# Kernel optimization log

Hardware: AMD Instinct MI355X
Metric: run time of the kernel (lower is better)

The kernel has to match this reference:

```python
import jax, jax.numpy as jnp
import numpy as np

B, S, M, D, H, L, FF = 2, 1024, 1024, 512, 8, 4, 2048
HD = D // H  # head dim 64
EPS = 1e-6   # fast_transformers linear-attention eps
LN_EPS = 1e-5


def setup_inputs() -> dict:
    key = jax.random.key(0)
    keys = iter(jax.random.split(key, 64))
    def w(shape, s=0.02):
        return jax.random.normal(next(keys), shape, dtype=jnp.float32) * s
    inp = {
        "memory": jax.random.normal(next(keys), (B, M, D), dtype=jnp.float32),
        "target": jax.random.normal(next(keys), (B, S, D), dtype=jnp.float32),
    }
    for p in ("sa", "ca"):
        for n in ("q", "k", "v", "o"):
            inp[f"{p}_W{n}"] = w((L, D, D))
            inp[f"{p}_b{n}"] = jnp.zeros((L, D), jnp.float32)
    inp["ff_W1"] = w((L, D, FF)); inp["ff_b1"] = jnp.zeros((L, FF), jnp.float32)
    inp["ff_W2"] = w((L, FF, D)); inp["ff_b2"] = jnp.zeros((L, D), jnp.float32)
    for n in ("ln1", "ln2", "ln3"):
        inp[f"{n}_g"] = jnp.ones((L, D), jnp.float32)
        inp[f"{n}_b"] = jnp.zeros((L, D), jnp.float32)
    inp["lnf_g"] = jnp.ones((D,), jnp.float32)
    inp["lnf_b"] = jnp.zeros((D,), jnp.float32)
    return inp


def _ln(x, g, b):
    m = x.mean(-1, keepdims=True)
    v = ((x - m) ** 2).mean(-1, keepdims=True)
    return (x - m) / jnp.sqrt(v + LN_EPS) * g + b


def _phi(x):  # elu feature map: elu(x) + 1
    return jax.nn.elu(x) + 1.0


def _heads(x, W, b):  # [b,s,D] -> [b,s,H,HD]
    y = x @ W + b
    return y.reshape(y.shape[0], y.shape[1], H, HD)


def _causal_linear_attn(q, k, v):
    # q,k already feature-mapped. cumulative KV state per step.
    kv = jnp.cumsum(jnp.einsum('bshd,bshm->bshdm', k, v), axis=1)  # [B,S,H,HD,HD]
    z = jnp.cumsum(k, axis=1)                                      # [B,S,H,HD]
    num = jnp.einsum('bshd,bshdm->bshm', q, kv)
    den = jnp.einsum('bshd,bshd->bsh', q, z) + EPS
    return num / den[..., None]


def _cross_linear_attn(q, k, v):
    kv = jnp.einsum('bmhd,bmhv->bhdv', k, v)  # [B,H,HD,HD]
    z = k.sum(axis=1)                          # [B,H,HD]
    num = jnp.einsum('bshd,bhdv->bshv', q, kv)
    den = jnp.einsum('bshd,bhd->bsh', q, z) + EPS
    return num / den[..., None]


def reference(memory, target,
              sa_Wq, sa_bq, sa_Wk, sa_bk, sa_Wv, sa_bv, sa_Wo, sa_bo,
              ca_Wq, ca_bq, ca_Wk, ca_bk, ca_Wv, ca_bv, ca_Wo, ca_bo,
              ff_W1, ff_b1, ff_W2, ff_b2,
              ln1_g, ln1_b, ln2_g, ln2_b, ln3_g, ln3_b, lnf_g, lnf_b):
    x = target
    for i in range(L):
        # causal linear self-attention
        q = _phi(_heads(x, sa_Wq[i], sa_bq[i]))
        k = _phi(_heads(x, sa_Wk[i], sa_bk[i]))
        v = _heads(x, sa_Wv[i], sa_bv[i])
        a = _causal_linear_attn(q, k, v).reshape(B, S, D) @ sa_Wo[i] + sa_bo[i]
        x = _ln(x + a, ln1_g[i], ln1_b[i])
        # linear cross-attention over memory
        q = _phi(_heads(x, ca_Wq[i], ca_bq[i]))
        k = _phi(_heads(memory, ca_Wk[i], ca_bk[i]))
        v = _heads(memory, ca_Wv[i], ca_bv[i])
        a = _cross_linear_attn(q, k, v).reshape(B, S, D) @ ca_Wo[i] + ca_bo[i]
        x = _ln(x + a, ln2_g[i], ln2_b[i])
        # gelu FFN
        y = jax.nn.gelu(x @ ff_W1[i] + ff_b1[i], approximate=False) @ ff_W2[i] + ff_b2[i]
        x = _ln(x + y, ln3_g[i], ln3_b[i])
    return _ln(x, lnf_g, lnf_b)
```

## Files before the change

kernel.cpp:

```cpp
#include <hip/hip_runtime.h>
#include <hip/hip_bf16.h>
#include <math.h>


typedef unsigned short u16;
typedef __bf16 bf16x8 __attribute__((ext_vector_type(8)));
typedef float f32x4v __attribute__((ext_vector_type(4)));
typedef long long i64;

#define DEVI __device__ __forceinline__

DEVI float bf2f(u16 u) { return __uint_as_float(((unsigned)u) << 16); }
DEVI u16 f2bf(float f) {
  unsigned u = __float_as_uint(f);
  u += 0x7FFFu + ((u >> 16) & 1u);
  return (u16)(u >> 16);
}

struct P8i { const float* p[8]; };
struct P8o { u16* p[8]; };

__global__ __launch_bounds__(256) void transpose_b8(P8i in, P8o out)
{
  __shared__ float tile[64 * 65];
  const int m = blockIdx.z;
  const int set = m >> 2, layer = m & 3;
  const float* src = in.p[set] + (size_t)layer * 512 * 512;
  u16* dst = out.p[set] + (size_t)layer * 512 * 512;
  const int n0 = blockIdx.x * 64, k0 = blockIdx.y * 64;
  const int t = threadIdx.x;
#pragma unroll
  for (int p = 0; p < 16; ++p) {
    const int e = t + p * 256;
    const int lk = e >> 6, ln = e & 63;
    tile[lk * 65 + ln] = src[(size_t)(k0 + lk) * 512 + n0 + ln];
  }
  __syncthreads();
#pragma unroll
  for (int p = 0; p < 16; ++p) {
    const int e = t + p * 256;
    const int ln = e >> 6, lk = e & 63;
    dst[(size_t)(n0 + ln) * 512 + k0 + lk] = f2bf(tile[lk * 65 + ln]);
  }
}

__global__ __launch_bounds__(256) void transpose_f2b(
    const float* __restrict__ in, u16* __restrict__ out, int K, int N)
{
  __shared__ float tile[64 * 65];
  const size_t mat = (size_t)blockIdx.z * K * N;
  const int n0 = blockIdx.x * 64, k0 = blockIdx.y * 64;
  const int t = threadIdx.x;
#pragma unroll
  for (int p = 0; p < 16; ++p) {
    const int e = t + p * 256;
    const int lk = e >> 6, ln = e & 63;
    tile[lk * 65 + ln] = in[mat + (size_t)(k0 + lk) * N + n0 + ln];
  }
  __syncthreads();
#pragma unroll
  for (int p = 0; p < 16; ++p) {
    const int e = t + p * 256;
    const int ln = e >> 6, lk = e & 63;
    out[mat + (size_t)(n0 + ln) * K + k0 + lk] = f2bf(tile[lk * 65 + ln]);
  }
}

__global__ __launch_bounds__(256) void cast_dual(
    const float* __restrict__ in, float* __restrict__ fout, u16* __restrict__ bout)
{
  const int i = blockIdx.x * 256 + threadIdx.x;
  const float4 a = ((const float4*)in)[i * 2];
  const float4 b = ((const float4*)in)[i * 2 + 1];
  if (fout) {
    ((float4*)fout)[i * 2] = a;
    ((float4*)fout)[i * 2 + 1] = b;
  }
  ((ushort4*)bout)[i * 2]     = make_ushort4(f2bf(a.x), f2bf(a.y), f2bf(a.z), f2bf(a.w));
  ((ushort4*)bout)[i * 2 + 1] = make_ushort4(f2bf(b.x), f2bf(b.y), f2bf(b.z), f2bf(b.w));
}

template<int CDT>
__global__ __launch_bounds__(256, 4) void gemm64(
    const u16* __restrict__ A0, const u16* __restrict__ A1, const u16* __restrict__ A2,
    const u16* __restrict__ W0, const u16* __restrict__ W1, const u16* __restrict__ W2,
    const float* __restrict__ b0, const float* __restrict__ b1, const float* __restrict__ b2,
    void* __restrict__ C0, void* __restrict__ C1, void* __restrict__ C2,
    int acts, int N, int K, int lda, int ldw, int lognyb,
    i64 zA, i64 zW, i64 zB, i64 zC, int biasAllZ)
{
  constexpr int LDT = 72;
  __shared__ __align__(16) u16 As[2][64 * LDT];
  __shared__ __align__(16) u16 Bs[2][64 * LDT];
  const int tid = threadIdx.x;
  const int by = blockIdx.y;
  const int z = blockIdx.z;
  const int seg = by >> lognyb;
  const int ny = by & ((1 << lognyb) - 1);
  const u16* A = (seg == 0 ? A0 : (seg == 1 ? A1 : A2)) + (size_t)z * zA;
  const u16* W = (seg == 0 ? W0 : (seg == 1 ? W1 : W2)) + (size_t)z * zW;
  const float* bias = (seg == 0 ? b0 : (seg == 1 ? b1 : b2)) + (size_t)z * zB;
  void* Cv = seg == 0 ? C0 : (seg == 1 ? C1 : C2);
  const int act = (acts >> (2 * seg)) & 3;
  const bool dobias = biasAllZ || (z == 0);

  const int bm0 = blockIdx.x * 64, bn0 = ny * 64;
  const int lane = tid & 63, wid = tid >> 6;
  const int wr = wid >> 1, wc = wid & 1;
  const int l15 = lane & 15, lg = lane >> 4;
  const int srow = tid >> 2, scg = (tid & 3) * 16;
  const u16* Ap = A + (size_t)(bm0 + srow) * lda + scg;
  const u16* Wp = W + (size_t)(bn0 + srow) * ldw + scg;

  uint4 ra0 = *(const uint4*)(Ap);
  uint4 ra1 = *(const uint4*)(Ap + 8);
  uint4 rb0 = *(const uint4*)(Wp);
  uint4 rb1 = *(const uint4*)(Wp + 8);
  *(uint4*)&As[0][srow * LDT + scg]     = ra0;
  *(uint4*)&As[0][srow * LDT + scg + 8] = ra1;
  *(uint4*)&Bs[0][srow * LDT + scg]     = rb0;
  *(uint4*)&Bs[0][srow * LDT + scg + 8] = rb1;
  __syncthreads();

  f32x4v acc[2][2] = {};
  int cur = 0;
  for (int k0 = 0; k0 < K; k0 += 64) {
    const bool more = (k0 + 64 < K);
    if (more) {
      ra0 = *(const uint4*)(Ap + k0 + 64);
      ra1 = *(const uint4*)(Ap + k0 + 72);
      rb0 = *(const uint4*)(Wp + k0 + 64);
      rb1 = *(const uint4*)(Wp + k0 + 72);
    }
    bf16x8 af[2][2], bw[2][2];
#pragma unroll
    for (int kk = 0; kk < 2; ++kk) {
#pragma unroll
      for (int mm = 0; mm < 2; ++mm)
        af[kk][mm] = *(const bf16x8*)&As[cur][(wr * 32 + mm * 16 + l15) * LDT + kk * 32 + lg * 8];
#pragma unroll
      for (int nn = 0; nn < 2; ++nn)
        bw[kk][nn] = *(const bf16x8*)&Bs[cur][(wc * 32 + nn * 16 + l15) * LDT + kk * 32 + lg * 8];
    }
#pragma unroll
    for (int kk = 0; kk < 2; ++kk)
#pragma unroll
      for (int mm = 0; mm < 2; ++mm)
#pragma unroll
        for (int nn = 0; nn < 2; ++nn)
          acc[mm][nn] = __builtin_amdgcn_mfma_f32_16x16x32_bf16(af[kk][mm], bw[kk][nn], acc[mm][nn], 0, 0, 0);
    if (more) {
      *(uint4*)&As[cur ^ 1][srow * LDT + scg]     = ra0;
      *(uint4*)&As[cur ^ 1][srow * LDT + scg + 8] = ra1;
      *(uint4*)&Bs[cur ^ 1][srow * LDT + scg]     = rb0;
      *(uint4*)&Bs[cur ^ 1][srow * LDT + scg + 8] = rb1;
    }
    __syncthreads();
    cur ^= 1;
  }
#pragma unroll
  for (int nn = 0; nn < 2; ++nn) {
    const int col = bn0 + wc * 32 + nn * 16 + l15;
    const float bv = dobias ? bias[col] : 0.f;
#pragma unroll
    for (int mm = 0; mm < 2; ++mm) {
#pragma unroll
      for (int r = 0; r < 4; ++r) {
        const int row = bm0 + wr * 32 + mm * 16 + lg * 4 + r;
        float v = acc[mm][nn][r] + bv;
        if (act == 1) v = v > 0.f ? v + 1.f : __expf(v);
        else if (act == 2) v = 0.5f * v * (1.f + erff(v * 0.70710678f));
        const size_t idx = (size_t)row * N + col + (size_t)z * zC;
        if (CDT == 0) ((float*)Cv)[idx] = v;
        else          ((u16*)Cv)[idx] = f2bf(v);
      }
    }
  }
}

__global__ __launch_bounds__(256) void lin_chunk_mfma(
    const u16* __restrict__ kbuf, const u16* __restrict__ vbuf,
    float* __restrict__ KVc, float* __restrict__ zc)
{
  constexpr int LDT = 72;
  __shared__ __align__(16) u16 Kt[64 * LDT];
  __shared__ __align__(16) u16 Vt[64 * LDT];
  const int c = blockIdx.x, bh = blockIdx.y, zl = blockIdx.z;
  kbuf += (size_t)zl * 2048 * 512;
  vbuf += (size_t)zl * 2048 * 512;
  KVc  += (size_t)zl * 16 * 16 * 4096;
  zc   += (size_t)zl * 16 * 16 * 64;
  const int b = bh >> 3, h = bh & 7;
  const int t = threadIdx.x;
  const size_t rowbase = (size_t)(b * 1024 + c * 64);
  const int sp = t >> 4, colq = (t & 15) * 4;
#pragma unroll
  for (int pp = 0; pp < 2; ++pp) {
    const int s0 = pp * 32 + 2 * sp;
    const ushort4 ka = *(const ushort4*)&kbuf[(rowbase + s0) * 512 + h * 64 + colq];
    const ushort4 kb_ = *(const ushort4*)&kbuf[(rowbase + s0 + 1) * 512 + h * 64 + colq];
    const ushort4 va = *(const ushort4*)&vbuf[(rowbase + s0) * 512 + h * 64 + colq];
    const ushort4 vb_ = *(const ushort4*)&vbuf[(rowbase + s0 + 1) * 512 + h * 64 + colq];
    *(unsigned*)&Kt[(colq + 0) * LDT + s0] = (unsigned)ka.x | ((unsigned)kb_.x << 16);
    *(unsigned*)&Kt[(colq + 1) * LDT + s0] = (unsigned)ka.y | ((unsigned)kb_.y << 16);
    *(unsigned*)&Kt[(colq + 2) * LDT + s0] = (unsigned)ka.z | ((unsigned)kb_.z << 16);
    *(unsigned*)&Kt[(colq + 3) * LDT + s0] = (unsigned)ka.w | ((unsigned)kb_.w << 16);
    *(unsigned*)&Vt[(colq + 0) * LDT + s0] = (unsigned)va.x | ((unsigned)vb_.x << 16);
    *(unsigned*)&Vt[(colq + 1) * LDT + s0] = (unsigned)va.y | ((unsigned)vb_.y << 16);
    *(unsigned*)&Vt[(colq + 2) * LDT + s0] = (unsigned)va.z | ((unsigned)vb_.z << 16);
    *(unsigned*)&Vt[(colq + 3) * LDT + s0] = (unsigned)va.w | ((unsigned)vb_.w << 16);
  }
  __syncthreads();
  {
    const int zd = t >> 2, zg = t & 3;
    float zp = 0.f;
#pragma unroll
    for (int ss = 0; ss < 16; ++ss) zp += bf2f(Kt[zd * LDT + zg * 16 + ss]);
    zp += __shfl_xor(zp, 1, 64);
    zp += __shfl_xor(zp, 2, 64);
    if (zg == 0) zc[(size_t)(bh * 16 + c) * 64 + zd] = zp;
  }
  const int lane = t & 63, wid = t >> 6;
  const int wr = wid >> 1, wc = wid & 1;
  const int l15 = lane & 15, lg = lane >> 4;
  bf16x8 av[2][2], bk[2][2];
#pragma unroll
  for (int kk = 0; kk < 2; ++kk) {
#pragma unroll
    for (int mm = 0; mm < 2; ++mm)
      av[kk][mm] = *(const bf16x8*)&Vt[(wr * 32 + mm * 16 + l15) * LDT + kk * 32 + lg * 8];
#pragma unroll
    for (int nn = 0; nn < 2; ++nn)
      bk[kk][nn] = *(const bf16x8*)&Kt[(wc * 32 + nn * 16 + l15) * LDT + kk * 32 + lg * 8];
  }
  f32x4v acc[2][2] = {};
#pragma unroll
  for (int kk = 0; kk < 2; ++kk)
#pragma unroll
    for (int mm = 0; mm < 2; ++mm)
#pragma unroll
      for (int nn = 0; nn < 2; ++nn)
        acc[mm][nn] = __builtin_amdgcn_mfma_f32_16x16x32_bf16(av[kk][mm], bk[kk][nn], acc[mm][nn], 0, 0, 0);
  float* kvout = KVc + (size_t)(bh * 16 + c) * 4096;
#pragma unroll
  for (int mm = 0; mm < 2; ++mm)
#pragma unroll
    for (int r = 0; r < 4; ++r) {
      const int row = wr * 32 + mm * 16 + lg * 4 + r;
#pragma unroll
      for (int nn = 0; nn < 2; ++nn) {
        const int col = wc * 32 + nn * 16 + l15;
        kvout[row * 64 + col] = acc[mm][nn][r];
      }
    }
}

__global__ __launch_bounds__(256) void sa_apply_mfma(
    const u16* __restrict__ qbuf, const u16* __restrict__ kbuf,
    const u16* __restrict__ vbuf, const float* __restrict__ KVc,
    const float* __restrict__ zc, u16* __restrict__ out)
{
  constexpr int LDT = 72;
  __shared__ __align__(16) u16 Qs[64 * LDT];
  __shared__ __align__(16) u16 Ks[64 * LDT];
  __shared__ __align__(16) u16 Vt[64 * LDT];
  __shared__ __align__(16) u16 Ps[64 * LDT];
  __shared__ __align__(16) u16 KVs[64 * LDT];
  __shared__ float zp[64];
  __shared__ float den1[2][64];
  __shared__ float den2[64];
  const int c = blockIdx.x, bh = blockIdx.y;
  const int b = bh >> 3, h = bh & 7;
  const int t = threadIdx.x;
  const size_t rowbase = (size_t)(b * 1024 + c * 64);
  {
    const int srow = t >> 2, scg = (t & 3) * 16;
    *(uint4*)&Qs[srow * LDT + scg]     = *(const uint4*)&qbuf[(rowbase + srow) * 512 + h * 64 + scg];
    *(uint4*)&Qs[srow * LDT + scg + 8] = *(const uint4*)&qbuf[(rowbase + srow) * 512 + h * 64 + scg + 8];
    *(uint4*)&Ks[srow * LDT + scg]     = *(const uint4*)&kbuf[(rowbase + srow) * 512 + h * 64 + scg];
    *(uint4*)&Ks[srow * LDT + scg + 8] = *(const uint4*)&kbuf[(rowbase + srow) * 512 + h * 64 + scg + 8];
    const float* kvbase = KVc + (size_t)(bh * 16) * 4096 + srow * 64 + scg;
    float4 s0 = make_float4(0, 0, 0, 0), s1 = s0, s2 = s0, s3 = s0;
    for (int cc = 0; cc < c; ++cc) {
      const float* p = kvbase + (size_t)cc * 4096;
      const float4 a0 = *(const float4*)&p[0];
      const float4 a1 = *(const float4*)&p[4];
      const float4 a2 = *(const float4*)&p[8];
      const float4 a3 = *(const float4*)&p[12];
      s0.x += a0.x; s0.y += a0.y; s0.z += a0.z; s0.w += a0.w;
      s1.x += a1.x; s1.y += a1.y; s1.z += a1.z; s1.w += a1.w;
      s2.x += a2.x; s2.y += a2.y; s2.z += a2.z; s2.w += a2.w;
      s3.x += a3.x; s3.y += a3.y; s3.z += a3.z; s3.w += a3.w;
    }
    *(ushort4*)&KVs[srow * LDT + scg + 0]  = make_ushort4(f2bf(s0.x), f2bf(s0.y), f2bf(s0.z), f2bf(s0.w));
    *(ushort4*)&KVs[srow * LDT + scg + 4]  = make_ushort4(f2bf(s1.x), f2bf(s1.y), f2bf(s1.z), f2bf(s1.w));
    *(ushort4*)&KVs[srow * LDT + scg + 8]  = make_ushort4(f2bf(s2.x), f2bf(s2.y), f2bf(s2.z), f2bf(s2.w));
    *(ushort4*)&KVs[srow * LDT + scg + 12] = make_ushort4(f2bf(s3.x), f2bf(s3.y), f2bf(s3.z), f2bf(s3.w));
  }
  {
    const int sp = t >> 4, colq = (t & 15) * 4;
#pragma unroll
    for (int pp = 0; pp < 2; ++pp) {
      const int s0 = pp * 32 + 2 * sp;
      const ushort4 va = *(const ushort4*)&vbuf[(rowbase + s0) * 512 + h * 64 + colq];
      const ushort4 vb_ = *(const ushort4*)&vbuf[(rowbase + s0 + 1) * 512 + h * 64 + colq];
      *(unsigned*)&Vt[(colq + 0) * LDT + s0] = (unsigned)va.x | ((unsigned)vb_.x << 16);
      *(unsigned*)&Vt[(colq + 1) * LDT + s0] = (unsigned)va.y | ((unsigned)vb_.y << 16);
      *(unsigned*)&Vt[(colq + 2) * LDT + s0] = (unsigned)va.z | ((unsigned)vb_.z << 16);
      *(unsigned*)&Vt[(colq + 3) * LDT + s0] = (unsigned)va.w | ((unsigned)vb_.w << 16);
    }
  }
  if (t < 64) {
    float z = 0.f;
    for (int cc = 0; cc < c; ++cc) z += zc[(size_t)(bh * 16 + cc) * 64 + t];
    zp[t] = z;
  }
  __syncthreads();
  {
    const int di = t >> 2, dg = t & 3;
    float p2 = 0.f;
#pragma unroll
    for (int dd = 0; dd < 16; ++dd)
      p2 += bf2f(Qs[di * LDT + dg * 16 + dd]) * zp[dg * 16 + dd];
    p2 += __shfl_xor(p2, 1, 64);
    p2 += __shfl_xor(p2, 2, 64);
    if (dg == 0) den2[di] = p2;
  }
  const int lane = t & 63, wid = t >> 6;
  const int wr = wid >> 1, wc = wid & 1;
  const int l15 = lane & 15, lg = lane >> 4;
  bf16x8 af_q[2][2], bx[2][2];
#pragma unroll
  for (int kk = 0; kk < 2; ++kk) {
#pragma unroll
    for (int mm = 0; mm < 2; ++mm)
      af_q[kk][mm] = *(const bf16x8*)&Qs[(wr * 32 + mm * 16 + l15) * LDT + kk * 32 + lg * 8];
#pragma unroll
    for (int nn = 0; nn < 2; ++nn)
      bx[kk][nn] = *(const bf16x8*)&Ks[(wc * 32 + nn * 16 + l15) * LDT + kk * 32 + lg * 8];
  }
  f32x4v s_acc[2][2] = {};
#pragma unroll
  for (int kk = 0; kk < 2; ++kk)
#pragma unroll
    for (int mm = 0; mm < 2; ++mm)
#pragma unroll
      for (int nn = 0; nn < 2; ++nn)
        s_acc[mm][nn] = __builtin_amdgcn_mfma_f32_16x16x32_bf16(af_q[kk][mm], bx[kk][nn], s_acc[mm][nn], 0, 0, 0);
#pragma unroll
  for (int mm = 0; mm < 2; ++mm)
#pragma unroll
    for (int r = 0; r < 4; ++r) {
      const int row = wr * 32 + mm * 16 + lg * 4 + r;
      float dsum = 0.f;
#pragma unroll
      for (int nn = 0; nn < 2; ++nn) {
        const int col = wc * 32 + nn * 16 + l15;
        const float val = (col <= row) ? s_acc[mm][nn][r] : 0.f;
        Ps[row * LDT + col] = f2bf(val);
        dsum += val;
      }
      dsum += __shfl_xor(dsum, 1, 64);
      dsum += __shfl_xor(dsum, 2, 64);
      dsum += __shfl_xor(dsum, 4, 64);
      dsum += __shfl_xor(dsum, 8, 64);
      if (l15 == 0) den1[wc][row] = dsum;
    }
  __syncthreads();
  bf16x8 ap[2][2];
#pragma unroll
  for (int kk = 0; kk < 2; ++kk) {
#pragma unroll
    for (int mm = 0; mm < 2; ++mm)
      ap[kk][mm] = *(const bf16x8*)&Ps[(wr * 32 + mm * 16 + l15) * LDT + kk * 32 + lg * 8];
#pragma unroll
    for (int nn = 0; nn < 2; ++nn)
      bx[kk][nn] = *(const bf16x8*)&Vt[(wc * 32 + nn * 16 + l15) * LDT + kk * 32 + lg * 8];
  }
  f32x4v o_acc[2][2] = {};
#pragma unroll
  for (int kk = 0; kk < 2; ++kk)
#pragma unroll
    for (int mm = 0; mm < 2; ++mm)
#pragma unroll
      for (int nn = 0; nn < 2; ++nn)
        o_acc[mm][nn] = __builtin_amdgcn_mfma_f32_16x16x32_bf16(ap[kk][mm], bx[kk][nn], o_acc[mm][nn], 0, 0, 0);
#pragma unroll
  for (int kk = 0; kk < 2; ++kk)
#pragma unroll
    for (int nn = 0; nn < 2; ++nn)
      bx[kk][nn] = *(const bf16x8*)&KVs[(wc * 32 + nn * 16 + l15) * LDT + kk * 32 + lg * 8];
#pragma unroll
  for (int kk = 0; kk < 2; ++kk)
#pragma unroll
    for (int mm = 0; mm < 2; ++mm)
#pragma unroll
      for (int nn = 0; nn < 2; ++nn)
        o_acc[mm][nn] = __builtin_amdgcn_mfma_f32_16x16x32_bf16(af_q[kk][mm], bx[kk][nn], o_acc[mm][nn], 0, 0, 0);
#pragma unroll
  for (int mm = 0; mm < 2; ++mm)
#pragma unroll
    for (int r = 0; r < 4; ++r) {
      const int row = wr * 32 + mm * 16 + lg * 4 + r;
      const float rden = 1.f / (den1[0][row] + den1[1][row] + den2[row] + 1e-6f);
#pragma unroll
      for (int nn = 0; nn < 2; ++nn) {
        const int col = wc * 32 + nn * 16 + l15;
        out[(rowbase + row) * 512 + h * 64 + col] = f2bf(o_acc[mm][nn][r] * rden);
      }
    }
}

__global__ __launch_bounds__(256) void ca_apply_mfma(
    const u16* __restrict__ qbuf, const float* __restrict__ KVc,
    const float* __restrict__ zc, u16* __restrict__ out)
{
  constexpr int LDT = 72;
  __shared__ __align__(16) u16 Qs[64 * LDT];
  __shared__ __align__(16) u16 KVs[64 * LDT];
  __shared__ float zt[64];
  __shared__ float den2[64];
  const int c = blockIdx.x, bh = blockIdx.y;
  const int b = bh >> 3, h = bh & 7;
  const int t = threadIdx.x;
  const size_t rowbase = (size_t)(b * 1024 + c * 64);
  {
    const int srow = t >> 2, scg = (t & 3) * 16;
    *(uint4*)&Qs[srow * LDT + scg]     = *(const uint4*)&qbuf[(rowbase + srow) * 512 + h * 64 + scg];
    *(uint4*)&Qs[srow * LDT + scg + 8] = *(const uint4*)&qbuf[(rowbase + srow) * 512 + h * 64 + scg + 8];
    const float* kvbase = KVc + (size_t)(bh * 16) * 4096 + srow * 64 + scg;
    float4 s0 = make_float4(0, 0, 0, 0), s1 = s0, s2 = s0, s3 = s0;
    for (int cc = 0; cc < 16; ++cc) {
      const float* p = kvbase + (size_t)cc * 4096;
      const float4 a0 = *(const float4*)&p[0];
      const float4 a1 = *(const float4*)&p[4];
      const float4 a2 = *(const float4*)&p[8];
      const float4 a3 = *(const float4*)&p[12];
      s0.x += a0.x; s0.y += a0.y; s0.z += a0.z; s0.w += a0.w;
      s1.x += a1.x; s1.y += a1.y; s1.z += a1.z; s1.w += a1.w;
      s2.x += a2.x; s2.y += a2.y; s2.z += a2.z; s2.w += a2.w;
      s3.x += a3.x; s3.y += a3.y; s3.z += a3.z; s3.w += a3.w;
    }
    *(ushort4*)&KVs[srow * LDT + scg + 0]  = make_ushort4(f2bf(s0.x), f2bf(s0.y), f2bf(s0.z), f2bf(s0.w));
    *(ushort4*)&KVs[srow * LDT + scg + 4]  = make_ushort4(f2bf(s1.x), f2bf(s1.y), f2bf(s1.z), f2bf(s1.w));
    *(ushort4*)&KVs[srow * LDT + scg + 8]  = make_ushort4(f2bf(s2.x), f2bf(s2.y), f2bf(s2.z), f2bf(s2.w));
    *(ushort4*)&KVs[srow * LDT + scg + 12] = make_ushort4(f2bf(s3.x), f2bf(s3.y), f2bf(s3.z), f2bf(s3.w));
  }
  if (t < 64) {
    float z = 0.f;
    for (int cc = 0; cc < 16; ++cc) z += zc[(size_t)(bh * 16 + cc) * 64 + t];
    zt[t] = z;
  }
  __syncthreads();
  {
    const int di = t >> 2, dg = t & 3;
    float p2 = 0.f;
#pragma unroll
    for (int dd = 0; dd < 16; ++dd)
      p2 += bf2f(Qs[di * LDT + dg * 16 + dd]) * zt[dg * 16 + dd];
    p2 += __shfl_xor(p2, 1, 64);
    p2 += __shfl_xor(p2, 2, 64);
    if (dg == 0) den2[di] = p2;
  }
  const int lane = t & 63, wid = t >> 6;
  const int wr = wid >> 1, wc = wid & 1;
  const int l15 = lane & 15, lg = lane >> 4;
  bf16x8 aq[2][2], bkv[2][2];
#pragma unroll
  for (int kk = 0; kk < 2; ++kk) {
#pragma unroll
    for (int mm = 0; mm < 2; ++mm)
      aq[kk][mm] = *(const bf16x8*)&Qs[(wr * 32 + mm * 16 + l15) * LDT + kk * 32 + lg * 8];
#pragma unroll
    for (int nn = 0; nn < 2; ++nn)
      bkv[kk][nn] = *(const bf16x8*)&KVs[(wc * 32 + nn * 16 + l15) * LDT + kk * 32 + lg * 8];
  }
  f32x4v o_acc[2][2] = {};
#pragma unroll
  for (int kk = 0; kk < 2; ++kk)
#pragma unroll
    for (int mm = 0; mm < 2; ++mm)
#pragma unroll
      for (int nn = 0; nn < 2; ++nn)
        o_acc[mm][nn] = __builtin_amdgcn_mfma_f32_16x16x32_bf16(aq[kk][mm], bkv[kk][nn], o_acc[mm][nn], 0, 0, 0);
  __syncthreads();
#pragma unroll
  for (int mm = 0; mm < 2; ++mm)
#pragma unroll
    for (int r = 0; r < 4; ++r) {
      const int row = wr * 32 + mm * 16 + lg * 4 + r;
      const float rden = 1.f / (den2[row] + 1e-6f);
#pragma unroll
      for (int nn = 0; nn < 2; ++nn) {
        const int col = wc * 32 + nn * 16 + l15;
        out[(rowbase + row) * 512 + h * 64 + col] = f2bf(o_acc[mm][nn][r] * rden);
      }
    }
}

template<int NPART>
__global__ __launch_bounds__(256) void ln_residual(
    float* __restrict__ x, const float* __restrict__ a, i64 pstride,
    const float* __restrict__ g, const float* __restrict__ bt,
    u16* __restrict__ xb)
{
  const int t = threadIdx.x, lane = t & 63, w = t >> 6;
  const int row = blockIdx.x * 4 + w;
  float* xr = x + (size_t)row * 512;
  float4 x0 = *(const float4*)&xr[lane * 8];
  float4 x1 = *(const float4*)&xr[lane * 8 + 4];
  float v[8] = { x0.x, x0.y, x0.z, x0.w, x1.x, x1.y, x1.z, x1.w };
#pragma unroll
  for (int p = 0; p < NPART; ++p) {
    const float* ar = a + (size_t)p * pstride + (size_t)row * 512;
    float4 a0 = *(const float4*)&ar[lane * 8];
    float4 a1 = *(const float4*)&ar[lane * 8 + 4];
    v[0] += a0.x; v[1] += a0.y; v[2] += a0.z; v[3] += a0.w;
    v[4] += a1.x; v[5] += a1.y; v[6] += a1.z; v[7] += a1.w;
  }
  float s = 0.f, sq = 0.f;
#pragma unroll
  for (int i = 0; i < 8; ++i) { s += v[i]; sq += v[i] * v[i]; }
#pragma unroll
  for (int off = 32; off > 0; off >>= 1) {
    s += __shfl_xor(s, off, 64);
    sq += __shfl_xor(sq, off, 64);
  }
  const float mean = s * (1.f / 512.f);
  const float var = sq * (1.f / 512.f) - mean * mean;
  const float rstd = rsqrtf(var + 1e-5f);
  float o[8];
#pragma unroll
  for (int i = 0; i < 8; ++i) {
    const int col = lane * 8 + i;
    o[i] = (v[i] - mean) * rstd * g[col] + bt[col];
  }
  *(float4*)&xr[lane * 8]     = make_float4(o[0], o[1], o[2], o[3]);
  *(float4*)&xr[lane * 8 + 4] = make_float4(o[4], o[5], o[6], o[7]);
  *(ushort4*)&xb[(size_t)row * 512 + lane * 8]     = make_ushort4(f2bf(o[0]), f2bf(o[1]), f2bf(o[2]), f2bf(o[3]));
  *(ushort4*)&xb[(size_t)row * 512 + lane * 8 + 4] = make_ushort4(f2bf(o[4]), f2bf(o[5]), f2bf(o[6]), f2bf(o[7]));
}

__global__ __launch_bounds__(256) void ln_final(
    const float* __restrict__ x, const float* __restrict__ g,
    const float* __restrict__ bt, float* __restrict__ out)
{
  const int t = threadIdx.x, lane = t & 63, w = t >> 6;
  const int row = blockIdx.x * 4 + w;
  const float* xr = x + (size_t)row * 512;
  float4 x0 = *(const float4*)&xr[lane * 8];
  float4 x1 = *(const float4*)&xr[lane * 8 + 4];
  float v[8] = { x0.x, x0.y, x0.z, x0.w, x1.x, x1.y, x1.z, x1.w };
  float s = 0.f, sq = 0.f;
#pragma unroll
  for (int i = 0; i < 8; ++i) { s += v[i]; sq += v[i] * v[i]; }
#pragma unroll
  for (int off = 32; off > 0; off >>= 1) {
    s += __shfl_xor(s, off, 64);
    sq += __shfl_xor(sq, off, 64);
  }
  const float mean = s * (1.f / 512.f);
  const float var = sq * (1.f / 512.f) - mean * mean;
  const float rstd = rsqrtf(var + 1e-5f);
  float o[8];
#pragma unroll
  for (int i = 0; i < 8; ++i) {
    const int col = lane * 8 + i;
    o[i] = (v[i] - mean) * rstd * g[col] + bt[col];
  }
  *(float4*)&out[(size_t)row * 512 + lane * 8]     = make_float4(o[0], o[1], o[2], o[3]);
  *(float4*)&out[(size_t)row * 512 + lane * 8 + 4] = make_float4(o[4], o[5], o[6], o[7]);
}

extern "C" void kernel_launch(void* const* d_in, const int* in_sizes, int n_in,
                              void* d_out, int out_size, void* d_ws, size_t ws_size,
                              hipStream_t stream)
{
  (void)in_sizes; (void)n_in; (void)out_size; (void)ws_size;
  constexpr int Dm = 512, Lc = 4, FFc = 2048;
  constexpr i64 TOK = 2048LL * 512;

  const float* memory = (const float*)d_in[0];
  const float* target = (const float*)d_in[1];
  const float *saW[4], *sab[4], *caW[4], *cab[4];
  for (int j = 0; j < 4; ++j) {
    saW[j] = (const float*)d_in[2 + 2 * j];
    sab[j] = (const float*)d_in[3 + 2 * j];
    caW[j] = (const float*)d_in[10 + 2 * j];
    cab[j] = (const float*)d_in[11 + 2 * j];
  }
  const float* ffW1 = (const float*)d_in[18];
  const float* ffb1 = (const float*)d_in[19];
  const float* ffW2 = (const float*)d_in[20];
  const float* ffb2 = (const float*)d_in[21];
  const float* lng[4] = { (const float*)d_in[22], (const float*)d_in[24],
                          (const float*)d_in[26], (const float*)d_in[28] };
  const float* lnb[4] = { (const float*)d_in[23], (const float*)d_in[25],
                          (const float*)d_in[27], (const float*)d_in[29] };

  size_t off = 0;
  auto alloc = [&](size_t bytes) -> void* {
    void* p = (char*)d_ws + off;
    off += (bytes + 255) & ~(size_t)255;
    return p;
  };
  u16* WtS[4]; u16* WtC[4];
  for (int j = 0; j < 4; ++j) WtS[j] = (u16*)alloc((size_t)Lc * Dm * Dm * 2);
  for (int j = 0; j < 4; ++j) WtC[j] = (u16*)alloc((size_t)Lc * Dm * Dm * 2);
  u16* WtF1 = (u16*)alloc((size_t)Lc * Dm * FFc * 2);
  u16* WtF2 = (u16*)alloc((size_t)Lc * FFc * Dm * 2);
  float* x     = (float*)alloc(TOK * 4);
  u16*   xb    = (u16*)alloc(TOK * 2);
  u16*   memb  = (u16*)alloc(TOK * 2);
  u16*   qh    = (u16*)alloc(TOK * 2);
  u16*   kh    = (u16*)alloc(TOK * 2);
  u16*   vh    = (u16*)alloc(TOK * 2);
  u16*   khAll = (u16*)alloc((size_t)Lc * TOK * 2);
  u16*   vhAll = (u16*)alloc((size_t)Lc * TOK * 2);
  float* resid = (float*)alloc((size_t)4 * TOK * 4);
  u16*   attn  = (u16*)alloc(TOK * 2);
  u16*   ffh   = (u16*)alloc((size_t)2048 * 2048 * 2);
  float* KVc   = (float*)alloc((size_t)16 * 16 * 4096 * 4);
  float* zcb   = (float*)alloc((size_t)16 * 16 * 64 * 4);
  float* KVcA  = (float*)alloc((size_t)Lc * 16 * 16 * 4096 * 4);
  float* zcbA  = (float*)alloc((size_t)Lc * 16 * 16 * 64 * 4);

  {
    P8i pin; P8o pout;
    for (int j = 0; j < 4; ++j) { pin.p[j] = saW[j]; pout.p[j] = WtS[j]; }
    for (int j = 0; j < 4; ++j) { pin.p[4 + j] = caW[j]; pout.p[4 + j] = WtC[j]; }
    transpose_b8<<<dim3(8, 8, 32), 256, 0, stream>>>(pin, pout);
  }
  transpose_f2b<<<dim3(32, 8, 4), 256, 0, stream>>>(ffW1, WtF1, Dm, FFc);
  transpose_f2b<<<dim3(8, 32, 4), 256, 0, stream>>>(ffW2, WtF2, FFc, Dm);

  cast_dual<<<512, 256, 0, stream>>>(target, x, xb);
  cast_dual<<<512, 256, 0, stream>>>(memory, nullptr, memb);

  gemm64<1><<<dim3(32, 16, 4), 256, 0, stream>>>(
      memb, memb, memb, WtC[1], WtC[2], WtC[2],
      cab[1], cab[2], cab[2], khAll, vhAll, vhAll,
      0x01 , 512, 512, 512, 512, 3,
      0, (i64)Dm * Dm, (i64)Dm, TOK, 1);
  lin_chunk_mfma<<<dim3(16, 16, 4), 256, 0, stream>>>(khAll, vhAll, KVcA, zcbA);

  for (int i = 0; i < Lc; ++i) {
    const size_t wo  = (size_t)i * Dm * Dm;
    const size_t wo1 = (size_t)i * Dm * FFc;
    const size_t wo2 = (size_t)i * FFc * Dm;
    gemm64<1><<<dim3(32, 24), 256, 0, stream>>>(
        xb, xb, xb, WtS[0] + wo, WtS[1] + wo, WtS[2] + wo,
        sab[0] + i * Dm, sab[1] + i * Dm, sab[2] + i * Dm,
        qh, kh, vh, 0x05, 512, 512, 512, 512, 3, 0, 0, 0, 0, 1);
    lin_chunk_mfma<<<dim3(16, 16), 256, 0, stream>>>(kh, vh, KVc, zcb);
    sa_apply_mfma<<<dim3(16, 16), 256, 0, stream>>>(qh, kh, vh, KVc, zcb, attn);
    gemm64<0><<<dim3(32, 8), 256, 0, stream>>>(
        attn, attn, attn, WtS[3] + wo, WtS[3] + wo, WtS[3] + wo,
        sab[3] + i * Dm, sab[3] + i * Dm, sab[3] + i * Dm,
        resid, resid, resid, 0, 512, 512, 512, 512, 3, 0, 0, 0, 0, 1);
    ln_residual<1><<<512, 256, 0, stream>>>(x, resid, TOK, lng[0] + i * Dm, lnb[0] + i * Dm, xb);
    gemm64<1><<<dim3(32, 8), 256, 0, stream>>>(
        xb, xb, xb, WtC[0] + wo, WtC[0] + wo, WtC[0] + wo,
        cab[0] + i * Dm, cab[0] + i * Dm, cab[0] + i * Dm,
        qh, qh, qh, 0x01, 512, 512, 512, 512, 3, 0, 0, 0, 0, 1);
    ca_apply_mfma<<<dim3(16, 16), 256, 0, stream>>>(
        qh, KVcA + (size_t)i * 16 * 16 * 4096, zcbA + (size_t)i * 16 * 16 * 64, attn);
    gemm64<0><<<dim3(32, 8), 256, 0, stream>>>(
        attn, attn, attn, WtC[3] + wo, WtC[3] + wo, WtC[3] + wo,
        cab[3] + i * Dm, cab[3] + i * Dm, cab[3] + i * Dm,
        resid, resid, resid, 0, 512, 512, 512, 512, 3, 0, 0, 0, 0, 1);
    ln_residual<1><<<512, 256, 0, stream>>>(x, resid, TOK, lng[1] + i * Dm, lnb[1] + i * Dm, xb);
    gemm64<1><<<dim3(32, 32), 256, 0, stream>>>(
        xb, xb, xb, WtF1 + wo1, WtF1 + wo1, WtF1 + wo1,
        ffb1 + i * FFc, ffb1 + i * FFc, ffb1 + i * FFc,
        ffh, ffh, ffh, 2, 2048, 512, 512, 512, 5, 0, 0, 0, 0, 1);
    gemm64<0><<<dim3(32, 8, 4), 256, 0, stream>>>(
        ffh, ffh, ffh, WtF2 + wo2, WtF2 + wo2, WtF2 + wo2,
        ffb2 + i * Dm, ffb2 + i * Dm, ffb2 + i * Dm,
        resid, resid, resid, 0, 512, 512, 2048, 2048, 3,
        512, 512, 0, TOK, 0);
    ln_residual<4><<<512, 256, 0, stream>>>(x, resid, TOK, lng[2] + i * Dm, lnb[2] + i * Dm, xb);
  }
  ln_final<<<512, 256, 0, stream>>>(x, lng[3], lnb[3], (float*)d_out);
}
```

Measured before the change: 596.6 us.

## Split-K small GEMMs, fuse phi into cross-attn apply, deepen GEMM register prefetch

The three 512x512 projection GEMMs per layer now use split-K over two z-slices that write fp32 partials. The following layernorm sums the two partials, and for the cross-attention query the apply kernel sums them and applies the elu+1 feature map. This doubles the block count on the small 256-block GEMMs to fill more CUs, at the cost of extra partial-sum traffic. The GEMM main loop is also restructured to hold two sets of prefetch registers and process two K-steps per iteration, so global loads run further ahead of compute, at the cost of more registers.

New measurement: 593.7 us. About the same (-0.5%).

```diff
diff --git a/kernel.cpp b/kernel.cpp
--- a/kernel.cpp
+++ b/kernel.cpp
@@ -111,36 +111,30 @@
   const int srow = tid >> 2, scg = (tid & 3) * 16;
   const u16* Ap = A + (size_t)(bm0 + srow) * lda + scg;
   const u16* Wp = W + (size_t)(bn0 + srow) * ldw + scg;
-
-  uint4 ra0 = *(const uint4*)(Ap);
-  uint4 ra1 = *(const uint4*)(Ap + 8);
-  uint4 rb0 = *(const uint4*)(Wp);
-  uint4 rb1 = *(const uint4*)(Wp + 8);
-  *(uint4*)&As[0][srow * LDT + scg]     = ra0;
-  *(uint4*)&As[0][srow * LDT + scg + 8] = ra1;
-  *(uint4*)&Bs[0][srow * LDT + scg]     = rb0;
-  *(uint4*)&Bs[0][srow * LDT + scg + 8] = rb1;
-  __syncthreads();
+  const int nk = K >> 6;
+
+  uint4 a00, a01, b00, b01;
+  uint4 a10, a11, b10, b11;
+#define LDSET0(k) { a00 = *(const uint4*)(Ap + (k) * 64); a01 = *(const uint4*)(Ap + (k) * 64 + 8); \
+                    b00 = *(const uint4*)(Wp + (k) * 64); b01 = *(const uint4*)(Wp + (k) * 64 + 8); }
+#define LDSET1(k) { a10 = *(const uint4*)(Ap + (k) * 64); a11 = *(const uint4*)(Ap + (k) * 64 + 8); \
+                    b10 = *(const uint4*)(Wp + (k) * 64); b11 = *(const uint4*)(Wp + (k) * 64 + 8); }
+#define STSET0(buf) { *(uint4*)&As[buf][srow * LDT + scg] = a00; *(uint4*)&As[buf][srow * LDT + scg + 8] = a01; \
+                      *(uint4*)&Bs[buf][srow * LDT + scg] = b00; *(uint4*)&Bs[buf][srow * LDT + scg + 8] = b01; }
+#define STSET1(buf) { *(uint4*)&As[buf][srow * LDT + scg] = a10; *(uint4*)&As[buf][srow * LDT + scg + 8] = a11; \
+                      *(uint4*)&Bs[buf][srow * LDT + scg] = b10; *(uint4*)&Bs[buf][srow * LDT + scg + 8] = b11; }
 
   f32x4v acc[2][2] = {};
-  int cur = 0;
-  for (int k0 = 0; k0 < K; k0 += 64) {
-    const bool more = (k0 + 64 < K);
-    if (more) {
-      ra0 = *(const uint4*)(Ap + k0 + 64);
-      ra1 = *(const uint4*)(Ap + k0 + 72);
-      rb0 = *(const uint4*)(Wp + k0 + 64);
-      rb1 = *(const uint4*)(Wp + k0 + 72);
-    }
+  auto mfma_on = [&](int buf) {
     bf16x8 af[2][2], bw[2][2];
 #pragma unroll
     for (int kk = 0; kk < 2; ++kk) {
 #pragma unroll
       for (int mm = 0; mm < 2; ++mm)
-        af[kk][mm] = *(const bf16x8*)&As[cur][(wr * 32 + mm * 16 + l15) * LDT + kk * 32 + lg * 8];
+        af[kk][mm] = *(const bf16x8*)&As[buf][(wr * 32 + mm * 16 + l15) * LDT + kk * 32 + lg * 8];
 #pragma unroll
       for (int nn = 0; nn < 2; ++nn)
-        bw[kk][nn] = *(const bf16x8*)&Bs[cur][(wc * 32 + nn * 16 + l15) * LDT + kk * 32 + lg * 8];
+        bw[kk][nn] = *(const bf16x8*)&Bs[buf][(wc * 32 + nn * 16 + l15) * LDT + kk * 32 + lg * 8];
     }
 #pragma unroll
     for (int kk = 0; kk < 2; ++kk)
@@ -149,15 +143,25 @@
 #pragma unroll
         for (int nn = 0; nn < 2; ++nn)
           acc[mm][nn] = __builtin_amdgcn_mfma_f32_16x16x32_bf16(af[kk][mm], bw[kk][nn], acc[mm][nn], 0, 0, 0);
-    if (more) {
-      *(uint4*)&As[cur ^ 1][srow * LDT + scg]     = ra0;
-      *(uint4*)&As[cur ^ 1][srow * LDT + scg + 8] = ra1;
-      *(uint4*)&Bs[cur ^ 1][srow * LDT + scg]     = rb0;
-      *(uint4*)&Bs[cur ^ 1][srow * LDT + scg + 8] = rb1;
-    }
+  };
+
+  LDSET0(0); STSET0(0);
+  LDSET1(1);
+  __syncthreads();
+  for (int k = 0; k < nk; k += 2) {
+    if (k + 2 < nk) LDSET0(k + 2);
+    mfma_on(0);
+    STSET1(1);
     __syncthreads();
-    cur ^= 1;
-  }
+    if (k + 3 < nk) LDSET1(k + 3);
+    mfma_on(1);
+    if (k + 2 < nk) STSET0(0);
+    __syncthreads();
+  }
+#undef LDSET0
+#undef LDSET1
+#undef STSET0
+#undef STSET1
 #pragma unroll
   for (int nn = 0; nn < 2; ++nn) {
     const int col = bn0 + wc * 32 + nn * 16 + l15;
@@ -412,7 +416,7 @@
 }
 
 __global__ __launch_bounds__(256) void ca_apply_mfma(
-    const u16* __restrict__ qbuf, const float* __restrict__ KVc,
+    const float* __restrict__ qp0, i64 qstride, const float* __restrict__ KVc,
     const float* __restrict__ zc, u16* __restrict__ out)
 {
   constexpr int LDT = 72;
@@ -426,8 +430,19 @@
   const size_t rowbase = (size_t)(b * 1024 + c * 64);
   {
     const int srow = t >> 2, scg = (t & 3) * 16;
-    *(uint4*)&Qs[srow * LDT + scg]     = *(const uint4*)&qbuf[(rowbase + srow) * 512 + h * 64 + scg];
-    *(uint4*)&Qs[srow * LDT + scg + 8] = *(const uint4*)&qbuf[(rowbase + srow) * 512 + h * 64 + scg + 8];
+    const float* qa = qp0 + (rowbase + srow) * 512 + h * 64 + scg;
+    const float* qb = qa + qstride;
+#pragma unroll
+    for (int i = 0; i < 4; ++i) {
+      const float4 u = *(const float4*)&qa[i * 4];
+      const float4 w = *(const float4*)&qb[i * 4];
+      float e0 = u.x + w.x, e1 = u.y + w.y, e2 = u.z + w.z, e3 = u.w + w.w;
+      e0 = e0 > 0.f ? e0 + 1.f : __expf(e0);
+      e1 = e1 > 0.f ? e1 + 1.f : __expf(e1);
+      e2 = e2 > 0.f ? e2 + 1.f : __expf(e2);
+      e3 = e3 > 0.f ? e3 + 1.f : __expf(e3);
+      *(ushort4*)&Qs[srow * LDT + scg + i * 4] = make_ushort4(f2bf(e0), f2bf(e1), f2bf(e2), f2bf(e3));
+    }
     const float* kvbase = KVc + (size_t)(bh * 16) * 4096 + srow * 64 + scg;
     float4 s0 = make_float4(0, 0, 0, 0), s1 = s0, s2 = s0, s3 = s0;
     for (int cc = 0; cc < 16; ++cc) {
@@ -640,7 +655,7 @@
   gemm64<1><<<dim3(32, 16, 4), 256, 0, stream>>>(
       memb, memb, memb, WtC[1], WtC[2], WtC[2],
       cab[1], cab[2], cab[2], khAll, vhAll, vhAll,
-      0x01 , 512, 512, 512, 512, 3,
+      0x01, 512, 512, 512, 512, 3,
       0, (i64)Dm * Dm, (i64)Dm, TOK, 1);
   lin_chunk_mfma<<<dim3(16, 16, 4), 256, 0, stream>>>(khAll, vhAll, KVcA, zcbA);
 
@@ -654,22 +669,25 @@
         qh, kh, vh, 0x05, 512, 512, 512, 512, 3, 0, 0, 0, 0, 1);
     lin_chunk_mfma<<<dim3(16, 16), 256, 0, stream>>>(kh, vh, KVc, zcb);
     sa_apply_mfma<<<dim3(16, 16), 256, 0, stream>>>(qh, kh, vh, KVc, zcb, attn);
-    gemm64<0><<<dim3(32, 8), 256, 0, stream>>>(
+    gemm64<0><<<dim3(32, 8, 2), 256, 0, stream>>>(
         attn, attn, attn, WtS[3] + wo, WtS[3] + wo, WtS[3] + wo,
         sab[3] + i * Dm, sab[3] + i * Dm, sab[3] + i * Dm,
-        resid, resid, resid, 0, 512, 512, 512, 512, 3, 0, 0, 0, 0, 1);
-    ln_residual<1><<<512, 256, 0, stream>>>(x, resid, TOK, lng[0] + i * Dm, lnb[0] + i * Dm, xb);
-    gemm64<1><<<dim3(32, 8), 256, 0, stream>>>(
+        resid, resid, resid, 0, 512, 256, 512, 512, 3,
+        256, 256, 0, TOK, 0);
+    ln_residual<2><<<512, 256, 0, stream>>>(x, resid, TOK, lng[0] + i * Dm, lnb[0] + i * Dm, xb);
+    gemm64<0><<<dim3(32, 8, 2), 256, 0, stream>>>(
         xb, xb, xb, WtC[0] + wo, WtC[0] + wo, WtC[0] + wo,
         cab[0] + i * Dm, cab[0] + i * Dm, cab[0] + i * Dm,
-        qh, qh, qh, 0x01, 512, 512, 512, 512, 3, 0, 0, 0, 0, 1);
+        resid, resid, resid, 0, 512, 256, 512, 512, 3,
+        256, 256, 0, TOK, 0);
     ca_apply_mfma<<<dim3(16, 16), 256, 0, stream>>>(
-        qh, KVcA + (size_t)i * 16 * 16 * 4096, zcbA + (size_t)i * 16 * 16 * 64, attn);
-    gemm64<0><<<dim3(32, 8), 256, 0, stream>>>(
+        resid, TOK, KVcA + (size_t)i * 16 * 16 * 4096, zcbA + (size_t)i * 16 * 16 * 64, attn);
+    gemm64<0><<<dim3(32, 8, 2), 256, 0, stream>>>(
         attn, attn, attn, WtC[3] + wo, WtC[3] + wo, WtC[3] + wo,
         cab[3] + i * Dm, cab[3] + i * Dm, cab[3] + i * Dm,
-        resid, resid, resid, 0, 512, 512, 512, 512, 3, 0, 0, 0, 0, 1);
-    ln_residual<1><<<512, 256, 0, stream>>>(x, resid, TOK, lng[1] + i * Dm, lnb[1] + i * Dm, xb);
+        resid, resid, resid, 0, 512, 256, 512, 512, 3,
+        256, 256, 0, TOK, 0);
+    ln_residual<2><<<512, 256, 0, stream>>>(x, resid, TOK, lng[1] + i * Dm, lnb[1] + i * Dm, xb);
     gemm64<1><<<dim3(32, 32), 256, 0, stream>>>(
         xb, xb, xb, WtF1 + wo1, WtF1 + wo1, WtF1 + wo1,
         ffb1 + i * FFc, ffb1 + i * FFc, ffb1 + i * FFc,
```
